# Kernel tuning notes

Measured on AMD Instinct MI355X. Metric: run time of the kernel, lower is better.

The kernel has to match this reference:

```python
import jax, jax.numpy as jnp
import numpy as np

DIM = 1024
HEADS = 16
HEAD_DIM = DIM // HEADS
SCALE = HEAD_DIM ** -0.5


def setup_inputs() -> dict:
    key = jax.random.key(0)
    ks = jax.random.split(key, 8)
    B, N, C = 2, 2048, DIM
    std = 0.02
    return {
        "x": jax.random.normal(ks[0], (B, N, C), dtype=jnp.float32),
        "e": jax.random.normal(ks[1], (B, N, C), dtype=jnp.float32),
        "W_qkv": jax.random.normal(ks[2], (C, 3 * C), dtype=jnp.float32) * std,
        "W_s": jax.random.normal(ks[3], (C, C), dtype=jnp.float32) * std,
        "W_gate": jax.random.normal(ks[4], (C, C), dtype=jnp.float32) * std,
        "W_proj": jax.random.normal(ks[5], (C, C), dtype=jnp.float32) * std,
        "b_proj": jax.random.normal(ks[6], (C,), dtype=jnp.float32) * std,
    }


def reference(x, e, W_qkv, W_s, W_gate, W_proj, b_proj):
    B, N, C = x.shape
    H, D = HEADS, HEAD_DIM
    # qkv: [B,N,3C] -> [3,B,H,N,D]
    qkv = (x @ W_qkv).reshape(B, N, 3, H, D).transpose(2, 0, 3, 1, 4)
    q, k, v = qkv[0], qkv[1], qkv[2]
    gate = x @ W_gate  # [B,N,C]
    # s bias fused into keys: [B,H,N,D]
    s = (e @ W_s).reshape(B, N, H, D).transpose(0, 2, 1, 3)
    attn = jnp.einsum("bhnd,bhmd->bhnm", q, k + s) * SCALE
    attn = jax.nn.softmax(attn, axis=-1)
    out = jnp.einsum("bhnm,bhmd->bhnd", attn, v)  # [B,H,N,D]
    out = out.transpose(0, 2, 1, 3).reshape(B, N, C)
    out = out * gate
    return out @ W_proj + b_proj
```

## Files before the change

### kernel.cpp

```cpp
#include <hip/hip_runtime.h>
#include <hip/hip_bf16.h>

#define SCALE 0.125f
#define QSCALE 0.18033688f
#define RESCALE_THR 8.0f

typedef __attribute__((ext_vector_type(8))) __bf16 bf16x8;
typedef __attribute__((ext_vector_type(4))) float f32x4;
typedef __attribute__((ext_vector_type(4))) short s16x4;
typedef __hip_bfloat16 bf16;

__device__ __forceinline__ void gl_lds16(const bf16* g, bf16* l) {
  __builtin_amdgcn_global_load_lds(
      (const __attribute__((address_space(1))) void*)g,
      (__attribute__((address_space(3))) void*)l, 16, 0, 0);
}

__device__ __forceinline__ float fexp2(float x) {
#if __has_builtin(__builtin_amdgcn_exp2f)
  return __builtin_amdgcn_exp2f(x);
#else
  return exp2f(x);
#endif
}

__device__ __forceinline__ unsigned cvt_pk_bf16(float lo, float hi) {
  unsigned r;
  asm("v_cvt_pk_bf16_f32 %0, %1, %2" : "=v"(r) : "v"(lo), "v"(hi));
  return r;
}

__device__ __forceinline__ f32x4 zf4() {
  f32x4 v; v[0] = 0.f; v[1] = 0.f; v[2] = 0.f; v[3] = 0.f; return v;
}

__global__ __launch_bounds__(256) void conv_bf16_k(const float* __restrict__ in,
                                                   bf16* __restrict__ out, int n4) {
  int i = blockIdx.x * 256 + threadIdx.x;
  if (i >= n4) return;
  const float4 v = reinterpret_cast<const float4*>(in)[i];
  union { bf16 h4[4]; s16x4 s; } u;
  u.h4[0] = __float2bfloat16(v.x);
  u.h4[1] = __float2bfloat16(v.y);
  u.h4[2] = __float2bfloat16(v.z);
  u.h4[3] = __float2bfloat16(v.w);
  reinterpret_cast<s16x4*>(out)[i] = u.s;
}

__global__ __launch_bounds__(256) void transp_k(const float* __restrict__ W,
                                                bf16* __restrict__ Wt, int K, int N) {
  __shared__ float t[32][33];
  const int tx = threadIdx.x, ty = threadIdx.y;
  const int n0 = blockIdx.x * 32, k0 = blockIdx.y * 32;
#pragma unroll
  for (int i = 0; i < 4; ++i)
    t[ty + 8 * i][tx] = W[(k0 + ty + 8 * i) * N + n0 + tx];
  __syncthreads();
#pragma unroll
  for (int i = 0; i < 4; ++i)
    Wt[(n0 + ty + 8 * i) * K + k0 + tx] = __float2bfloat16(t[tx][ty + 8 * i]);
}

struct GemmP {
  const bf16* A;
  const bf16* B0;
  const bf16* B1;
  const bf16* sT;
  bf16 *q, *k, *vt, *gate, *obf;
  float* out;
  const float* bias;
};

template <int EPI>
__global__ __launch_bounds__(256) void gemm_k(GemmP p) {
  constexpr int K = 1024;
  __shared__ bf16 As[128 * 32];
  __shared__ bf16 Bs[128 * 32];
  const int tid = threadIdx.x;
  const int wid = tid >> 6, lane = tid & 63;
  const int l15 = lane & 15, l4 = lane >> 4;
  const int wr = wid >> 1, wc = wid & 1;
  const int m0 = blockIdx.y * 128, n0 = blockIdx.x * 128;
  const bf16* Arow = p.A + m0 * K;
  const bf16* Brow;
  if (EPI == 1 && n0 >= 3072) Brow = p.B1 + (n0 - 3072) * K;
  else Brow = p.B0 + n0 * K;

  f32x4 acc[4][4];
#pragma unroll
  for (int m = 0; m < 4; ++m)
#pragma unroll
    for (int n = 0; n < 4; ++n) acc[m][n] = zf4();

  const int srow = tid >> 2, skc = tid & 3;
  for (int kt = 0; kt < K; kt += 32) {
#pragma unroll
    for (int it = 0; it < 2; ++it) {
      gl_lds16(Arow + (it * 64 + srow) * K + kt + skc * 8, As + it * 2048 + wid * 512);
      gl_lds16(Brow + (it * 64 + srow) * K + kt + skc * 8, Bs + it * 2048 + wid * 512);
    }
    __syncthreads();
    bf16x8 af[4], bfr[4];
#pragma unroll
    for (int m = 0; m < 4; ++m)
      af[m] = *reinterpret_cast<const bf16x8*>(&As[(wr * 64 + m * 16 + l15) * 32 + 8 * l4]);
#pragma unroll
    for (int n = 0; n < 4; ++n)
      bfr[n] = *reinterpret_cast<const bf16x8*>(&Bs[(wc * 64 + n * 16 + l15) * 32 + 8 * l4]);
#pragma unroll
    for (int m = 0; m < 4; ++m)
#pragma unroll
      for (int n = 0; n < 4; ++n)
        acc[m][n] = __builtin_amdgcn_mfma_f32_16x16x32_bf16(af[m], bfr[n], acc[m][n], 0, 0, 0);
    __syncthreads();
  }

#pragma unroll
  for (int m = 0; m < 4; ++m) {
    const int gr0 = m0 + wr * 64 + m * 16 + l4 * 4;
    const int bb = gr0 >> 11;
    const int nn0 = gr0 & 2047;
#pragma unroll
    for (int n = 0; n < 4; ++n) {
      const int gc = n0 + wc * 64 + n * 16 + l15;
      if (EPI == 1) {
        if (gc < 3072) {
          const int t = gc >> 10, hd = gc & 1023;
          const int h = hd >> 6, d = hd & 63;
          const int base = ((bb * 16 + h) * 2048 + nn0) * 64 + d;
          if (t == 0) {
#pragma unroll
            for (int r = 0; r < 4; ++r)
              p.q[base + r * 64] = __float2bfloat16(acc[m][n][r] * QSCALE);
          } else if (t == 1) {
#pragma unroll
            for (int r = 0; r < 4; ++r)
              p.k[base + r * 64] =
                  __float2bfloat16(acc[m][n][r] + __bfloat162float(p.sT[base + r * 64]));
          } else {
            union { bf16 h4[4]; s16x4 s; } u;
#pragma unroll
            for (int r = 0; r < 4; ++r) u.h4[r] = __float2bfloat16(acc[m][n][r]);
            *reinterpret_cast<s16x4*>(&p.vt[((bb * 16 + h) * 64 + d) * 2048 + nn0]) = u.s;
          }
        } else {
          const int gcc = gc - 3072;
#pragma unroll
          for (int r = 0; r < 4; ++r)
            p.gate[(gr0 + r) * 1024 + gcc] = __float2bfloat16(acc[m][n][r]);
        }
      }
    }
  }
}

template <int EPI>
__global__ __launch_bounds__(256) void gemm2_k(GemmP p) {
  constexpr int K = 1024;
  __shared__ bf16 As[64 * 32];
  __shared__ bf16 Bs[128 * 32];
  const int tid = threadIdx.x;
  const int wid = tid >> 6, lane = tid & 63;
  const int l15 = lane & 15, l4 = lane >> 4;
  const int wc = wid;
  const int m0 = blockIdx.y * 64, n0 = blockIdx.x * 128;
  const bf16* Arow = p.A + m0 * K;
  const bf16* Brow = p.B0 + n0 * K;

  f32x4 acc[4][2];
#pragma unroll
  for (int m = 0; m < 4; ++m)
#pragma unroll
    for (int n = 0; n < 2; ++n) acc[m][n] = zf4();

  const int srowA = tid >> 2, skc = tid & 3;
  for (int kt = 0; kt < K; kt += 32) {
    gl_lds16(Arow + srowA * K + kt + skc * 8, As + wid * 512);
#pragma unroll
    for (int it = 0; it < 2; ++it)
      gl_lds16(Brow + (it * 64 + srowA) * K + kt + skc * 8, Bs + it * 2048 + wid * 512);
    __syncthreads();
    bf16x8 af[4], bfr[2];
#pragma unroll
    for (int m = 0; m < 4; ++m)
      af[m] = *reinterpret_cast<const bf16x8*>(&As[(m * 16 + l15) * 32 + 8 * l4]);
#pragma unroll
    for (int n = 0; n < 2; ++n)
      bfr[n] = *reinterpret_cast<const bf16x8*>(&Bs[(wc * 32 + n * 16 + l15) * 32 + 8 * l4]);
#pragma unroll
    for (int m = 0; m < 4; ++m)
#pragma unroll
      for (int n = 0; n < 2; ++n)
        acc[m][n] = __builtin_amdgcn_mfma_f32_16x16x32_bf16(af[m], bfr[n], acc[m][n], 0, 0, 0);
    __syncthreads();
  }

#pragma unroll
  for (int m = 0; m < 4; ++m) {
    const int gr0 = m0 + m * 16 + l4 * 4;
    const int bb = gr0 >> 11;
    const int nn0 = gr0 & 2047;
#pragma unroll
    for (int n = 0; n < 2; ++n) {
      const int gc = n0 + wc * 32 + n * 16 + l15;
      if (EPI == 0) {
        const int h = gc >> 6, d = gc & 63;
        bf16* dst = p.obf + ((bb * 16 + h) * 2048 + nn0) * 64 + d;
#pragma unroll
        for (int r = 0; r < 4; ++r) dst[r * 64] = __float2bfloat16(acc[m][n][r]);
      } else {
        const float bias = p.bias[gc];
#pragma unroll
        for (int r = 0; r < 4; ++r) p.out[(gr0 + r) * 1024 + gc] = acc[m][n][r] + bias;
      }
    }
  }
}

__global__ __launch_bounds__(256) void flash_k(const bf16* __restrict__ qT,
                                               const bf16* __restrict__ kTb,
                                               const bf16* __restrict__ vTt,
                                               const bf16* __restrict__ gateb,
                                               bf16* __restrict__ attng) {
  __shared__ bf16 Ks[2][64 * 64];
  __shared__ bf16 Vs[2][64 * 64];
  const int tid = threadIdx.x;
  const int wid = tid >> 6, lane = tid & 63;
  const int l15 = lane & 15, l4 = lane >> 4;
  const int hbit = lane >> 5;
  const int qt = blockIdx.x, bh = blockIdx.y;
  const int qr0 = qt * 64 + wid * 16;
  const bf16* qbase = qT + (bh * 2048 + qr0) * 64;
  const bf16x8 qf0 = *reinterpret_cast<const bf16x8*>(&qbase[l15 * 64 + 8 * l4]);
  const bf16x8 qf1 = *reinterpret_cast<const bf16x8*>(&qbase[l15 * 64 + 32 + 8 * l4]);
  const bf16* kbase = kTb + bh * 2048 * 64;
  const bf16* vbase = vTt + bh * 64 * 2048;
  const int srcQ0 = (((lane & 16) << 1) | (lane & 15)) << 2;
  const int srcQ1 = srcQ0 | 64;

  f32x4 o[4];
#pragma unroll
  for (int i = 0; i < 4; ++i) o[i] = zf4();
  float mrun = -1e30f, lrun = 0.f;
  const int srow = tid >> 3, sc = tid & 7;

  auto stage = [&](int b, int kt) {
#pragma unroll
    for (int it = 0; it < 2; ++it) {
      const int row = it * 32 + srow;
      const int c2 = sc ^ (row & 7);
      gl_lds16(kbase + (kt * 64 + row) * 64 + c2 * 8, &Ks[b][it * 2048 + wid * 512]);
      gl_lds16(vbase + row * 2048 + kt * 64 + c2 * 8, &Vs[b][it * 2048 + wid * 512]);
    }
  };

  stage(0, 0);
  __syncthreads();
  int cur = 0;

  for (int kt = 0; kt < 32; ++kt) {
    if (kt < 31) stage(cur ^ 1, kt + 1);

    f32x4 sa[4];
#pragma unroll
    for (int n = 0; n < 4; ++n) sa[n] = zf4();
    __builtin_amdgcn_s_setprio(1);
#pragma unroll
    for (int kk = 0; kk < 2; ++kk) {
      const bf16x8 qv = kk ? qf1 : qf0;
#pragma unroll
      for (int n = 0; n < 4; ++n) {
        const int key = n * 16 + l15;
        const bf16x8 kv = *reinterpret_cast<const bf16x8*>(
            &Ks[cur][key * 64 + ((kk * 4 + l4) ^ (key & 7)) * 8]);
        sa[n] = __builtin_amdgcn_mfma_f32_16x16x32_bf16(kv, qv, sa[n], 0, 0, 0);
      }
    }
    __builtin_amdgcn_s_setprio(0);

    float mt = sa[0][0];
#pragma unroll
    for (int n = 0; n < 4; ++n)
#pragma unroll
      for (int r = 0; r < 4; ++r) mt = fmaxf(mt, sa[n][r]);
    mt = fmaxf(mt, __shfl_xor(mt, 16, 64));
    mt = fmaxf(mt, __shfl_xor(mt, 32, 64));

    const bool upd = !__all(mt <= mrun + RESCALE_THR);
    float fac = 1.f;
    if (upd) {
      const float mn = fmaxf(mrun, mt);
      fac = fexp2(mrun - mn);
      mrun = mn;
    }

    float p[4][4];
    float psum = 0.f;
#pragma unroll
    for (int n = 0; n < 4; ++n)
#pragma unroll
      for (int r = 0; r < 4; ++r) {
        p[n][r] = fexp2(sa[n][r] - mrun);
        psum += p[n][r];
      }
    psum += __shfl_xor(psum, 16, 64);
    psum += __shfl_xor(psum, 32, 64);
    if (upd) {
      lrun = lrun * fac + psum;
#pragma unroll
      for (int nd = 0; nd < 4; ++nd)
#pragma unroll
        for (int r = 0; r < 4; ++r) o[nd][r] *= fac;
    } else {
      lrun += psum;
    }

    int Cp[4][2];
#pragma unroll
    for (int n = 0; n < 4; ++n) {
      Cp[n][0] = (int)cvt_pk_bf16(p[n][0], p[n][1]);
      Cp[n][1] = (int)cvt_pk_bf16(p[n][2], p[n][3]);
    }

    __builtin_amdgcn_s_setprio(1);
#pragma unroll
    for (int kk = 0; kk < 2; ++kk) {
      const int x0 = __builtin_amdgcn_ds_bpermute(srcQ0, Cp[2 * kk][0]);
      const int x1 = __builtin_amdgcn_ds_bpermute(srcQ0, Cp[2 * kk + 1][0]);
      const int y0 = __builtin_amdgcn_ds_bpermute(srcQ0, Cp[2 * kk][1]);
      const int y1 = __builtin_amdgcn_ds_bpermute(srcQ0, Cp[2 * kk + 1][1]);
      const int z0 = __builtin_amdgcn_ds_bpermute(srcQ1, Cp[2 * kk][0]);
      const int z1 = __builtin_amdgcn_ds_bpermute(srcQ1, Cp[2 * kk + 1][0]);
      const int t0 = __builtin_amdgcn_ds_bpermute(srcQ1, Cp[2 * kk][1]);
      const int t1 = __builtin_amdgcn_ds_bpermute(srcQ1, Cp[2 * kk + 1][1]);
      union { int u[4]; bf16x8 v; } pw;
      pw.u[0] = hbit ? x1 : x0;
      pw.u[1] = hbit ? y1 : y0;
      pw.u[2] = hbit ? z1 : z0;
      pw.u[3] = hbit ? t1 : t0;
#pragma unroll
      for (int nd = 0; nd < 4; ++nd) {
        const int d = nd * 16 + l15;
        const bf16x8 vv = *reinterpret_cast<const bf16x8*>(
            &Vs[cur][d * 64 + ((kk * 4 + l4) ^ (d & 7)) * 8]);
        o[nd] = __builtin_amdgcn_mfma_f32_16x16x32_bf16(vv, pw.v, o[nd], 0, 0, 0);
      }
    }
    __builtin_amdgcn_s_setprio(0);

    __syncthreads();
    cur ^= 1;
  }

  const int bb = bh >> 4, h = bh & 15;
  const int grow = bb * 2048 + qr0 + l15;
  const float inv = 1.0f / lrun;
#pragma unroll
  for (int nd = 0; nd < 4; ++nd) {
    const int gi = grow * 1024 + h * 64 + nd * 16 + l4 * 4;
    union { s16x4 s; bf16 h4[4]; } gu, ou;
    gu.s = *reinterpret_cast<const s16x4*>(&gateb[gi]);
#pragma unroll
    for (int r = 0; r < 4; ++r)
      ou.h4[r] = __float2bfloat16(o[nd][r] * inv * __bfloat162float(gu.h4[r]));
    *reinterpret_cast<s16x4*>(&attng[gi]) = ou.s;
  }
}

extern "C" void kernel_launch(void* const* d_in, const int* in_sizes, int n_in,
                              void* d_out, int out_size, void* d_ws, size_t ws_size,
                              hipStream_t stream) {
  const float* x = (const float*)d_in[0];
  const float* e = (const float*)d_in[1];
  const float* Wqkv = (const float*)d_in[2];
  const float* Ws = (const float*)d_in[3];
  const float* Wgate = (const float*)d_in[4];
  const float* Wproj = (const float*)d_in[5];
  const float* bproj = (const float*)d_in[6];
  float* out = (float*)d_out;

  char* w = (char*)d_ws;
  auto carve = [&](size_t bytes) -> void* {
    void* p = (void*)w;
    w += (bytes + 255) & ~size_t(255);
    return p;
  };
  bf16* xbf    = (bf16*)carve(4096UL * 1024 * 2);
  bf16* ebf    = (bf16*)carve(4096UL * 1024 * 2);
  bf16* Wqkvt  = (bf16*)carve(3072UL * 1024 * 2);
  bf16* Wst    = (bf16*)carve(1024UL * 1024 * 2);
  bf16* Wgatet = (bf16*)carve(1024UL * 1024 * 2);
  bf16* Wprojt = (bf16*)carve(1024UL * 1024 * 2);
  bf16* kTb    = (bf16*)carve(32UL * 2048 * 64 * 2);
  bf16* vTt    = (bf16*)carve(32UL * 64 * 2048 * 2);
  bf16* sT     = (bf16*)carve(32UL * 2048 * 64 * 2);
  bf16* gateb  = (bf16*)carve(4096UL * 1024 * 2);
  bf16* qT     = ebf;
  bf16* attng  = sT;

  conv_bf16_k<<<4096, 256, 0, stream>>>(x, xbf, 1048576);
  conv_bf16_k<<<4096, 256, 0, stream>>>(e, ebf, 1048576);
  transp_k<<<dim3(96, 32), dim3(32, 8), 0, stream>>>(Wqkv, Wqkvt, 1024, 3072);
  transp_k<<<dim3(32, 32), dim3(32, 8), 0, stream>>>(Ws, Wst, 1024, 1024);
  transp_k<<<dim3(32, 32), dim3(32, 8), 0, stream>>>(Wgate, Wgatet, 1024, 1024);
  transp_k<<<dim3(32, 32), dim3(32, 8), 0, stream>>>(Wproj, Wprojt, 1024, 1024);

  GemmP ps{};
  ps.A = ebf; ps.B0 = Wst; ps.obf = sT;
  gemm2_k<0><<<dim3(8, 64), 256, 0, stream>>>(ps);

  GemmP pq{};
  pq.A = xbf; pq.B0 = Wqkvt; pq.B1 = Wgatet; pq.sT = sT;
  pq.q = qT; pq.k = kTb; pq.vt = vTt; pq.gate = gateb;
  gemm_k<1><<<dim3(32, 32), 256, 0, stream>>>(pq);

  flash_k<<<dim3(32, 32), 256, 0, stream>>>(qT, kTb, vTt, gateb, attng);

  GemmP pp{};
  pp.A = attng; pp.B0 = Wprojt; pp.out = out; pp.bias = bproj;
  gemm2_k<2><<<dim3(8, 64), 256, 0, stream>>>(pp);
}
```

Before: 302.3 us.

## Rewrite QKV+gate GEMM with 256x256 tiles, double-buffered swizzled LDS and grid remap

Replaces the 128x128 single-buffered QKV/gate GEMM with a 512-thread 256x256-tile kernel that uses K=64 steps, double-buffered LDS loaded via global_load_lds, and XOR-swizzled LDS layout to avoid bank conflicts. Next-tile loads are issued while MFMAs run, with setprio raising priority for the MFMA phases, and block IDs are remapped for better L2 locality. This aims to increase data reuse per tile and overlap memory with compute, at the cost of 128KB LDS per block, high register pressure and a small grid (256 blocks).

```diff
diff --git a/kernel.cpp b/kernel.cpp
--- a/kernel.cpp
+++ b/kernel.cpp
@@ -71,84 +71,128 @@
   const float* bias;
 };
 
-template <int EPI>
-__global__ __launch_bounds__(256) void gemm_k(GemmP p) {
+__global__ __launch_bounds__(512, 2) void gemm256_k(GemmP p) {
   constexpr int K = 1024;
-  __shared__ bf16 As[128 * 32];
-  __shared__ bf16 Bs[128 * 32];
+  constexpr int NT = 16;
+  __shared__ bf16 AB[2][2][256 * 64];
   const int tid = threadIdx.x;
   const int wid = tid >> 6, lane = tid & 63;
   const int l15 = lane & 15, l4 = lane >> 4;
-  const int wr = wid >> 1, wc = wid & 1;
-  const int m0 = blockIdx.y * 128, n0 = blockIdx.x * 128;
-  const bf16* Arow = p.A + m0 * K;
-  const bf16* Brow;
-  if (EPI == 1 && n0 >= 3072) Brow = p.B1 + (n0 - 3072) * K;
-  else Brow = p.B0 + n0 * K;
-
-  f32x4 acc[4][4];
-#pragma unroll
-  for (int m = 0; m < 4; ++m)
+  const int wr = wid >> 2, wc = wid & 3;
+
+  const int bid0 = blockIdx.y * 16 + blockIdx.x;
+  const int bid = (bid0 & 7) * 32 + (bid0 >> 3);
+  const int m0 = (bid >> 4) * 256, n0 = (bid & 15) * 256;
+
+  const bf16* Arow = p.A + (size_t)m0 * K;
+  const bf16* Brow = (n0 >= 3072) ? p.B1 + (size_t)(n0 - 3072) * K
+                                  : p.B0 + (size_t)n0 * K;
+
+  f32x4 acc[8][4];
+#pragma unroll
+  for (int m = 0; m < 8; ++m)
 #pragma unroll
     for (int n = 0; n < 4; ++n) acc[m][n] = zf4();
 
-  const int srow = tid >> 2, skc = tid & 3;
-  for (int kt = 0; kt < K; kt += 32) {
-#pragma unroll
-    for (int it = 0; it < 2; ++it) {
-      gl_lds16(Arow + (it * 64 + srow) * K + kt + skc * 8, As + it * 2048 + wid * 512);
-      gl_lds16(Brow + (it * 64 + srow) * K + kt + skc * 8, Bs + it * 2048 + wid * 512);
-    }
-    __syncthreads();
-    bf16x8 af[4], bfr[4];
-#pragma unroll
-    for (int m = 0; m < 4; ++m)
-      af[m] = *reinterpret_cast<const bf16x8*>(&As[(wr * 64 + m * 16 + l15) * 32 + 8 * l4]);
-#pragma unroll
-    for (int n = 0; n < 4; ++n)
-      bfr[n] = *reinterpret_cast<const bf16x8*>(&Bs[(wc * 64 + n * 16 + l15) * 32 + 8 * l4]);
-#pragma unroll
-    for (int m = 0; m < 4; ++m)
-#pragma unroll
-      for (int n = 0; n < 4; ++n)
-        acc[m][n] = __builtin_amdgcn_mfma_f32_16x16x32_bf16(af[m], bfr[n], acc[m][n], 0, 0, 0);
-    __syncthreads();
-  }
-
-#pragma unroll
-  for (int m = 0; m < 4; ++m) {
-    const int gr0 = m0 + wr * 64 + m * 16 + l4 * 4;
+  const int srow = tid >> 3, sc = tid & 7;
+  auto stageA = [&](int b, int kt) {
+#pragma unroll
+    for (int s = 0; s < 4; ++s) {
+      const int r = s * 64 + srow;
+      const int c2 = sc ^ (r & 7);
+      gl_lds16(Arow + (size_t)r * K + kt * 64 + c2 * 8, &AB[b][0][r * 64 + sc * 8]);
+    }
+  };
+  auto stageB = [&](int b, int kt) {
+#pragma unroll
+    for (int s = 0; s < 4; ++s) {
+      const int r = s * 64 + srow;
+      const int c2 = sc ^ (r & 7);
+      gl_lds16(Brow + (size_t)r * K + kt * 64 + c2 * 8, &AB[b][1][r * 64 + sc * 8]);
+    }
+  };
+
+  stageA(0, 0);
+  stageB(0, 0);
+  __syncthreads();
+  int cur = 0;
+
+  for (int kt = 0; kt < NT; ++kt) {
+    bf16x8 bfv[4][2];
+#pragma unroll
+    for (int q = 0; q < 4; ++q) {
+      bf16x8 af[2][2];
+#pragma unroll
+      for (int mm = 0; mm < 2; ++mm) {
+        const int row = wr * 128 + (q * 2 + mm) * 16 + l15;
+#pragma unroll
+        for (int ks = 0; ks < 2; ++ks)
+          af[mm][ks] = *reinterpret_cast<const bf16x8*>(
+              &AB[cur][0][row * 64 + ((ks * 4 + l4) ^ (row & 7)) * 8]);
+      }
+      if (q == 0) {
+#pragma unroll
+        for (int n = 0; n < 4; ++n) {
+          const int row = wc * 64 + n * 16 + l15;
+#pragma unroll
+          for (int ks = 0; ks < 2; ++ks)
+            bfv[n][ks] = *reinterpret_cast<const bf16x8*>(
+                &AB[cur][1][row * 64 + ((ks * 4 + l4) ^ (row & 7)) * 8]);
+        }
+      }
+      if (q == 0 && kt + 1 < NT) stageA(cur ^ 1, kt + 1);
+      if (q == 1 && kt + 1 < NT) stageB(cur ^ 1, kt + 1);
+
+      __builtin_amdgcn_s_barrier();
+      __builtin_amdgcn_s_setprio(1);
+#pragma unroll
+      for (int mm = 0; mm < 2; ++mm)
+#pragma unroll
+        for (int n = 0; n < 4; ++n)
+#pragma unroll
+          for (int ks = 0; ks < 2; ++ks)
+            acc[q * 2 + mm][n] = __builtin_amdgcn_mfma_f32_16x16x32_bf16(
+                af[mm][ks], bfv[n][ks], acc[q * 2 + mm][n], 0, 0, 0);
+      __builtin_amdgcn_s_setprio(0);
+      __builtin_amdgcn_s_barrier();
+    }
+    asm volatile("s_waitcnt vmcnt(0)" ::: "memory");
+    __builtin_amdgcn_s_barrier();
+    cur ^= 1;
+  }
+
+#pragma unroll
+  for (int m = 0; m < 8; ++m) {
+    const int gr0 = m0 + wr * 128 + m * 16 + l4 * 4;
     const int bb = gr0 >> 11;
     const int nn0 = gr0 & 2047;
 #pragma unroll
     for (int n = 0; n < 4; ++n) {
       const int gc = n0 + wc * 64 + n * 16 + l15;
-      if (EPI == 1) {
-        if (gc < 3072) {
-          const int t = gc >> 10, hd = gc & 1023;
-          const int h = hd >> 6, d = hd & 63;
-          const int base = ((bb * 16 + h) * 2048 + nn0) * 64 + d;
-          if (t == 0) {
-#pragma unroll
-            for (int r = 0; r < 4; ++r)
-              p.q[base + r * 64] = __float2bfloat16(acc[m][n][r] * QSCALE);
-          } else if (t == 1) {
-#pragma unroll
-            for (int r = 0; r < 4; ++r)
-              p.k[base + r * 64] =
-                  __float2bfloat16(acc[m][n][r] + __bfloat162float(p.sT[base + r * 64]));
-          } else {
-            union { bf16 h4[4]; s16x4 s; } u;
-#pragma unroll
-            for (int r = 0; r < 4; ++r) u.h4[r] = __float2bfloat16(acc[m][n][r]);
-            *reinterpret_cast<s16x4*>(&p.vt[((bb * 16 + h) * 64 + d) * 2048 + nn0]) = u.s;
-          }
+      if (gc < 3072) {
+        const int t = gc >> 10, hd = gc & 1023;
+        const int h = hd >> 6, d = hd & 63;
+        const int base = ((bb * 16 + h) * 2048 + nn0) * 64 + d;
+        if (t == 0) {
+#pragma unroll
+          for (int r = 0; r < 4; ++r)
+            p.q[base + r * 64] = __float2bfloat16(acc[m][n][r] * QSCALE);
+        } else if (t == 1) {
+#pragma unroll
+          for (int r = 0; r < 4; ++r)
+            p.k[base + r * 64] =
+                __float2bfloat16(acc[m][n][r] + __bfloat162float(p.sT[base + r * 64]));
         } else {
-          const int gcc = gc - 3072;
-#pragma unroll
-          for (int r = 0; r < 4; ++r)
-            p.gate[(gr0 + r) * 1024 + gcc] = __float2bfloat16(acc[m][n][r]);
+          union { bf16 h4[4]; s16x4 s; } u;
+#pragma unroll
+          for (int r = 0; r < 4; ++r) u.h4[r] = __float2bfloat16(acc[m][n][r]);
+          *reinterpret_cast<s16x4*>(&p.vt[((bb * 16 + h) * 64 + d) * 2048 + nn0]) = u.s;
         }
+      } else {
+        const int gcc = gc - 3072;
+#pragma unroll
+        for (int r = 0; r < 4; ++r)
+          p.gate[(gr0 + r) * 1024 + gcc] = __float2bfloat16(acc[m][n][r]);
       }
     }
   }
@@ -412,7 +456,7 @@
   GemmP pq{};
   pq.A = xbf; pq.B0 = Wqkvt; pq.B1 = Wgatet; pq.sT = sT;
   pq.q = qT; pq.k = kTb; pq.vt = vTt; pq.gate = gateb;
-  gemm_k<1><<<dim3(32, 32), 256, 0, stream>>>(pq);
+  gemm256_k<<<dim3(16, 16), 512, 0, stream>>>(pq);
 
   flash_k<<<dim3(32, 32), 256, 0, stream>>>(qT, kTb, vTt, gateb, attng);
 
```

New measurement: 279.7 us. -7.5%, faster.
